# Kernel optimization log

Measured on AMD Instinct MI355X. Metric: run time of the kernel, lower is better.

The kernel has to match this reference:

```python
import jax, jax.numpy as jnp
import numpy as np

NPOINTS = 1024
RADIUS = 0.2
NSAMPLE = 32


def setup_inputs() -> dict:
    key = jax.random.key(0)
    k1, k2, k3, k4 = jax.random.split(key, 4)
    return {
        "xyz_all": jax.random.uniform(k1, (4, 8192, 3), jnp.float32),
        "normals": jax.random.normal(k2, (4, 8192, 3), jnp.float32),
        "xyz_voxel": jax.random.uniform(k3, (4, 4096, 3), jnp.float32),
        "normals_voxel": jax.random.normal(k4, (4, 4096, 3), jnp.float32),
    }


def _fps(xyz, npoints):
    # Furthest point sampling over a single cloud. xyz: (n, 3) -> (npoints,) int32
    n = xyz.shape[0]

    def body(carry, _):
        dists, last = carry
        d = jnp.sum((xyz - xyz[last]) ** 2, axis=-1)      # (n,) dist^2 to last pick
        dists = jnp.minimum(dists, d)                      # running min dist to set
        nxt = jnp.argmax(dists).astype(jnp.int32)          # farthest point
        return (dists, nxt), nxt

    init = (jnp.full((n,), 1e10, xyz.dtype), jnp.int32(0))
    _, rest = jax.lax.scan(body, init, None, length=npoints - 1)
    return jnp.concatenate([jnp.zeros((1,), jnp.int32), rest])


def _ball_query(xyz, new_xyz, radius, nsample):
    # xyz: (N,3) cloud, new_xyz: (S,3) centers -> (S, nsample) int32 indices
    # squared distances via GEMM form (compute-friendly)
    d2 = (jnp.sum(new_xyz ** 2, -1)[:, None] + jnp.sum(xyz ** 2, -1)[None, :]
          - 2.0 * jnp.einsum('sc,nc->sn', new_xyz, xyz))   # (S, N)
    N = xyz.shape[0]
    cand = jnp.where(d2 < radius * radius, jnp.arange(N, dtype=jnp.int32), N)
    cand = jnp.sort(cand, axis=-1)[:, :nsample]            # first nsample in-ball indices
    first = cand[:, :1]
    idx = jnp.where(cand == N, first, cand)                # pad with first valid index
    return jnp.where(idx == N, 0, idx)                     # degenerate: empty ball -> 0


def reference(xyz_all, normals, xyz_voxel, normals_voxel):
    # FPS on voxel points
    fps_idx = jax.vmap(lambda p: _fps(p, NPOINTS))(xyz_voxel)                 # (B, S)
    new_xyz = jax.vmap(lambda p, i: p[i])(xyz_voxel, fps_idx)                 # (B, S, 3)
    new_normals = jax.vmap(lambda p, i: p[i])(normals_voxel, fps_idx)         # (B, S, 3)
    # Ball query on full cloud
    idx = jax.vmap(lambda p, q: _ball_query(p, q, RADIUS, NSAMPLE))(xyz_all, new_xyz)  # (B, S, ns)
    grouped_xyz = jax.vmap(lambda p, i: p[i])(xyz_all, idx)                   # (B, S, ns, 3)
    rel = grouped_xyz - new_xyz[:, :, None, :]                                # center-relative
    new_features = jnp.transpose(rel, (0, 3, 1, 2))                           # (B, 3, S, ns)
    grouped_n = jax.vmap(lambda f, i: f[i])(normals, idx)                     # (B, S, ns, C)
    new_features_normals = jnp.concatenate(
        [new_features, jnp.transpose(grouped_n, (0, 3, 1, 2))], axis=1)       # (B, 3+C, S, ns)
    return new_xyz, new_normals, new_features, new_features_normals
```

## Files before the change

kernel.cpp:

```cpp
#include <hip/hip_runtime.h>
#include <hip/hip_bf16.h>

#define B 4
#define N_ALL 8192
#define N_VOX 4096
#define S_PTS 1024
#define K_SAMPLE 32
#define R2 0.04f

#define FPS_T 256
#define NPAIR 8
#define PREP_BLOCKS ((B * N_ALL) / FPS_T)

typedef float vf2 __attribute__((ext_vector_type(2)));

__device__ __forceinline__ double mk_key(float v, unsigned int ilo) {
    return __longlong_as_double(
        ((unsigned long long)__float_as_uint(v) << 32) | ilo);
}

__device__ __forceinline__ double wave_key_max_f64(double k) {
    unsigned long long ku = __double_as_longlong(k);
#define DPP_RED(ctrl)                                                              \
    {                                                                              \
        unsigned int lo = (unsigned int)ku;                                        \
        unsigned int hi = (unsigned int)(ku >> 32);                                \
        unsigned int nlo =                                                         \
            (unsigned int)__builtin_amdgcn_update_dpp(0, (int)lo, ctrl, 0xf, 0xf, false); \
        unsigned int nhi =                                                         \
            (unsigned int)__builtin_amdgcn_update_dpp(0, (int)hi, ctrl, 0xf, 0xf, false); \
        double nk = __longlong_as_double(((unsigned long long)nhi << 32) | nlo);   \
        double cur = fmax(__longlong_as_double(ku), nk);                           \
        ku = __double_as_longlong(cur);                                            \
    }
    DPP_RED(0x111);
    DPP_RED(0x112);
    DPP_RED(0x114);
    DPP_RED(0x118);
    DPP_RED(0x142);
    DPP_RED(0x143);
#undef DPP_RED
    return __longlong_as_double(ku);
}

__global__ __launch_bounds__(FPS_T, 1) void fps_prep_kernel(
    const float* __restrict__ xyz_voxel,
    const float* __restrict__ normals_voxel,
    const float* __restrict__ xyz_all,
    float* __restrict__ out_xyz,
    float* __restrict__ out_normals,
    float4* __restrict__ ws_packed,
    int do_prep)
{
#pragma clang fp contract(off)
    if (blockIdx.x >= B) {
        if (!do_prep) return;
        int pid = (blockIdx.x - B) * FPS_T + threadIdx.x;
        if (pid < B * N_ALL) {
            float x = xyz_all[pid * 3 + 0];
            float y = xyz_all[pid * 3 + 1];
            float z = xyz_all[pid * 3 + 2];
            float pp = __fadd_rn(__fadd_rn(__fmul_rn(x, x), __fmul_rn(y, y)),
                                 __fmul_rn(z, z));
            ws_packed[pid] = make_float4(x, y, z, pp);
        }
        return;
    }

    const int b = blockIdx.x;
    const int t = threadIdx.x;
    const int wid = t >> 6;
    const int lane = t & 63;

    __shared__ float4 sp[N_VOX];
    __shared__ int fps_idx_s[S_PTS];
    __shared__ alignas(16) unsigned long long s_part[2][FPS_T / 64];

    const float* xyz = xyz_voxel + (size_t)b * N_VOX * 3;
    for (int i = t; i < N_VOX; i += FPS_T) {
        float x = xyz[i * 3 + 0];
        float y = xyz[i * 3 + 1];
        float z = xyz[i * 3 + 2];
        sp[i] = make_float4(x, y, z, 0.0f);
    }
    __syncthreads();

    vf2 px2[NPAIR], py2[NPAIR], pz2[NPAIR], dist2[NPAIR];
    unsigned int ilo[2 * NPAIR];
#pragma unroll
    for (int jp = 0; jp < NPAIR; jp++) {
        float4 a = sp[t + (2 * jp) * FPS_T];
        float4 c = sp[t + (2 * jp + 1) * FPS_T];
        px2[jp] = vf2{a.x, c.x};
        py2[jp] = vf2{a.y, c.y};
        pz2[jp] = vf2{a.z, c.z};
        dist2[jp] = vf2{1e10f, 1e10f};
        ilo[2 * jp]     = ~(unsigned int)((2 * jp) * FPS_T + t);
        ilo[2 * jp + 1] = ~(unsigned int)((2 * jp + 1) * FPS_T + t);
    }

    if (t == 0) fps_idx_s[0] = 0;
    float4 c0 = sp[0];
    float lx = c0.x, ly = c0.y, lz = c0.z;

    for (int step = 1; step < S_PTS; step++) {
        double kk[2 * NPAIR];
#pragma unroll
        for (int jp = 0; jp < NPAIR; jp++) {
            vf2 dx = px2[jp] - lx;
            vf2 dy = py2[jp] - ly;
            vf2 dz = pz2[jp] - lz;
            vf2 d = (dx * dx + dy * dy) + dz * dz;
            vf2 dm = dist2[jp];
            dm.x = fminf(dm.x, d.x);
            dm.y = fminf(dm.y, d.y);
            dist2[jp] = dm;
            kk[2 * jp]     = mk_key(dm.x, ilo[2 * jp]);
            kk[2 * jp + 1] = mk_key(dm.y, ilo[2 * jp + 1]);
        }
        double m0 = fmax(fmax(kk[0], kk[1]),   fmax(kk[2], kk[3]));
        double m1 = fmax(fmax(kk[4], kk[5]),   fmax(kk[6], kk[7]));
        double m2 = fmax(fmax(kk[8], kk[9]),   fmax(kk[10], kk[11]));
        double m3 = fmax(fmax(kk[12], kk[13]), fmax(kk[14], kk[15]));
        double a0 = fmax(fmax(m0, m1), fmax(m2, m3));
        a0 = wave_key_max_f64(a0);

        const int buf = step & 1;
        if (lane == 63)
            s_part[buf][wid] = (unsigned long long)__double_as_longlong(a0);
        __syncthreads();
        double2 q0 = *((const double2*)&s_part[buf][0]);
        double2 q1 = *((const double2*)&s_part[buf][2]);
        double p0 = fmax(fmax(q0.x, q0.y), fmax(q1.x, q1.y));
        int besti = (int)(~(unsigned int)(unsigned long long)__double_as_longlong(p0))
                    & (N_VOX - 1);
        float4 cb = sp[besti];
        lx = cb.x; ly = cb.y; lz = cb.z;
        if (t == 0) fps_idx_s[step] = besti;
    }
    __syncthreads();

    for (int i = t; i < S_PTS; i += FPS_T) {
        int idx = fps_idx_s[i];
        int o = (b * S_PTS + i) * 3;
        float4 c = sp[idx];
        out_xyz[o + 0] = c.x;
        out_xyz[o + 1] = c.y;
        out_xyz[o + 2] = c.z;
        const float* nv = normals_voxel + ((size_t)b * N_VOX + idx) * 3;
        out_normals[o + 0] = nv[0];
        out_normals[o + 1] = nv[1];
        out_normals[o + 2] = nv[2];
    }
}

template <bool PACKED>
__global__ __launch_bounds__(256) void ballquery_group_kernel(
    const float* __restrict__ xyz_all,
    const float* __restrict__ normals,
    const float* __restrict__ new_xyz,
    const float4* __restrict__ pw,
    float* __restrict__ out_feat,
    float* __restrict__ out_featn)
{
#pragma clang fp contract(off)
    const int wid = threadIdx.x >> 6;
    const int lane = threadIdx.x & 63;
    const int q = blockIdx.x * 4 + wid;
    const int b = q >> 10;
    const int s = q & 1023;

    const float* xyz = xyz_all + (size_t)b * N_ALL * 3;
    const float* nrm = normals + (size_t)b * N_ALL * 3;
    const float4* pwb = PACKED ? (pw + (size_t)b * N_ALL) : nullptr;

    const float qx = new_xyz[q * 3 + 0];
    const float qy = new_xyz[q * 3 + 1];
    const float qz = new_xyz[q * 3 + 2];
    const float qq = __fadd_rn(__fadd_rn(__fmul_rn(qx, qx), __fmul_rn(qy, qy)),
                               __fmul_rn(qz, qz));

    __shared__ int sidx[4][K_SAMPLE];

    int cnt = 0;
    if (PACKED) {
        for (int g = 0; g < N_ALL / 256 && cnt < K_SAMPLE; g++) {
            int base = g * 256 + lane;
            float4 c0 = pwb[base];
            float4 c1 = pwb[base + 64];
            float4 c2 = pwb[base + 128];
            float4 c3 = pwb[base + 192];
            vf2 pxA = vf2{c0.x, c1.x}, pxB = vf2{c2.x, c3.x};
            vf2 pyA = vf2{c0.y, c1.y}, pyB = vf2{c2.y, c3.y};
            vf2 pzA = vf2{c0.z, c1.z}, pzB = vf2{c2.z, c3.z};
            vf2 ppA = vf2{c0.w, c1.w}, ppB = vf2{c2.w, c3.w};
            vf2 dtA = qx * pxA; dtA = dtA + qy * pyA; dtA = dtA + qz * pzA;
            vf2 dtB = qx * pxB; dtB = dtB + qy * pyB; dtB = dtB + qz * pzB;
            vf2 d2A = (qq + ppA) - 2.0f * dtA;
            vf2 d2B = (qq + ppB) - 2.0f * dtB;
            float d2s[4] = {d2A.x, d2A.y, d2B.x, d2B.y};
#pragma unroll
            for (int u = 0; u < 4; u++) {
                bool hit = d2s[u] < R2;
                unsigned long long mask = __ballot(hit);
                if (hit) {
                    int pos = cnt + __popcll(mask & ((1ull << lane) - 1ull));
                    if (pos < K_SAMPLE) sidx[wid][pos] = g * 256 + u * 64 + lane;
                }
                cnt += (int)__popcll(mask);
            }
        }
    } else {
        for (int c = 0; c < N_ALL / 64 && cnt < K_SAMPLE; c++) {
            int i = c * 64 + lane;
            float px = xyz[i * 3 + 0];
            float py = xyz[i * 3 + 1];
            float pz = xyz[i * 3 + 2];
            float pp = __fadd_rn(__fadd_rn(__fmul_rn(px, px), __fmul_rn(py, py)),
                                 __fmul_rn(pz, pz));
            float dt = __fadd_rn(__fadd_rn(__fmul_rn(qx, px), __fmul_rn(qy, py)),
                                 __fmul_rn(qz, pz));
            float d2 = __fsub_rn(__fadd_rn(qq, pp), __fmul_rn(2.0f, dt));
            bool hit = d2 < R2;
            unsigned long long mask = __ballot(hit);
            if (hit) {
                int pos = cnt + __popcll(mask & ((1ull << lane) - 1ull));
                if (pos < K_SAMPLE) sidx[wid][pos] = i;
            }
            cnt += (int)__popcll(mask);
        }
    }
    __syncthreads();

    if (lane < K_SAMPLE) {
        int idxj;
        if (cnt == 0)        idxj = 0;
        else if (lane < cnt) idxj = sidx[wid][lane];
        else                 idxj = sidx[wid][0];

        float px, py, pz;
        if (PACKED) {
            float4 cc = pwb[idxj];
            px = cc.x; py = cc.y; pz = cc.z;
        } else {
            px = xyz[idxj * 3 + 0];
            py = xyz[idxj * 3 + 1];
            pz = xyz[idxj * 3 + 2];
        }
        float rx = __fsub_rn(px, qx);
        float ry = __fsub_rn(py, qy);
        float rz = __fsub_rn(pz, qz);

        int o3 = ((b * 3) * S_PTS + s) * K_SAMPLE + lane;
        out_feat[o3 + 0 * 32768] = rx;
        out_feat[o3 + 1 * 32768] = ry;
        out_feat[o3 + 2 * 32768] = rz;

        float nx = nrm[idxj * 3 + 0];
        float ny = nrm[idxj * 3 + 1];
        float nz = nrm[idxj * 3 + 2];

        int o4 = ((b * 6) * S_PTS + s) * K_SAMPLE + lane;
        out_featn[o4 + 0 * 32768] = rx;
        out_featn[o4 + 1 * 32768] = ry;
        out_featn[o4 + 2 * 32768] = rz;
        out_featn[o4 + 3 * 32768] = nx;
        out_featn[o4 + 4 * 32768] = ny;
        out_featn[o4 + 5 * 32768] = nz;
    }
}

extern "C" void kernel_launch(void* const* d_in, const int* in_sizes, int n_in,
                              void* d_out, int out_size, void* d_ws, size_t ws_size,
                              hipStream_t stream) {
    const float* xyz_all       = (const float*)d_in[0];
    const float* normals       = (const float*)d_in[1];
    const float* xyz_voxel     = (const float*)d_in[2];
    const float* normals_voxel = (const float*)d_in[3];

    float* out = (float*)d_out;
    float* out_xyz     = out;
    float* out_normals = out + 12288;
    float* out_feat    = out + 24576;
    float* out_featn   = out + 417792;

    const size_t need = (size_t)B * N_ALL * sizeof(float4);
    const bool use_ws = ws_size >= need;

    fps_prep_kernel<<<B + (use_ws ? PREP_BLOCKS : 0), FPS_T, 0, stream>>>(
        xyz_voxel, normals_voxel, xyz_all, out_xyz, out_normals,
        (float4*)d_ws, use_ws ? 1 : 0);

    if (use_ws) {
        ballquery_group_kernel<true><<<(B * S_PTS) / 4, 256, 0, stream>>>(
            xyz_all, normals, out_xyz, (const float4*)d_ws, out_feat, out_featn);
    } else {
        ballquery_group_kernel<false><<<(B * S_PTS) / 4, 256, 0, stream>>>(
            xyz_all, normals, out_xyz, nullptr, out_feat, out_featn);
    }
}
```

Baseline: 583.1 us.

## Fuse FPS and ball query into one producer-consumer kernel

```diff
diff --git a/kernel.cpp b/kernel.cpp
--- a/kernel.cpp
+++ b/kernel.cpp
@@ -1,5 +1,4 @@
 #include <hip/hip_runtime.h>
-#include <hip/hip_bf16.h>
 
 #define B 4
 #define N_ALL 8192
@@ -10,7 +9,8 @@
 
 #define FPS_T 256
 #define NPAIR 8
-#define PREP_BLOCKS ((B * N_ALL) / FPS_T)
+#define CONS_BLOCKS 256
+#define PUB_CHUNK 128
 
 typedef float vf2 __attribute__((ext_vector_type(2)));
 
@@ -43,38 +43,149 @@
     return __longlong_as_double(ku);
 }
 
-__global__ __launch_bounds__(FPS_T, 1) void fps_prep_kernel(
+template <bool WAIT>
+__device__ void consumer_body(
+    const int W,
+    const float* __restrict__ xyz_all,
+    const float* __restrict__ normals,
+    const float* __restrict__ xyz_voxel,
+    const float* __restrict__ normals_voxel,
+    float* __restrict__ out_xyz,
+    float* __restrict__ out_normals,
+    float* __restrict__ out_feat,
+    float* __restrict__ out_featn,
+    const int* __restrict__ g_idx,
+    const int* __restrict__ prog,
+    int (*__restrict__ sidx)[K_SAMPLE])
+{
+#pragma clang fp contract(off)
+    const int wid = threadIdx.x >> 6;
+    const int lane = threadIdx.x & 63;
+    const int s = W;
+
+    if constexpr (WAIT) {
+        const int need = s + 1;
+        for (int b = 0; b < B; b++) {
+            int cur;
+            while ((cur = __hip_atomic_load(&prog[b], __ATOMIC_RELAXED,
+                                            __HIP_MEMORY_SCOPE_AGENT)) < need) {
+                if (need - cur > 2 * PUB_CHUNK) __builtin_amdgcn_s_sleep(127);
+                else                            __builtin_amdgcn_s_sleep(32);
+            }
+        }
+        __threadfence();
+    }
+
+    for (int b = 0; b < B; b++) {
+        const float* xyz = xyz_all + (size_t)b * N_ALL * 3;
+        const float* nrm = normals + (size_t)b * N_ALL * 3;
+
+        float qx, qy, qz;
+        if constexpr (WAIT) {
+            const int idx = g_idx[b * S_PTS + s];
+            const float* pv = xyz_voxel + ((size_t)b * N_VOX + idx) * 3;
+            const float* nv = normals_voxel + ((size_t)b * N_VOX + idx) * 3;
+            qx = pv[0]; qy = pv[1]; qz = pv[2];
+            if (lane < 3) {
+                out_xyz[(b * S_PTS + s) * 3 + lane]     = pv[lane];
+                out_normals[(b * S_PTS + s) * 3 + lane] = nv[lane];
+            }
+        } else {
+            const float* pv = out_xyz + (b * S_PTS + s) * 3;
+            qx = pv[0]; qy = pv[1]; qz = pv[2];
+        }
+        const float qq = __fadd_rn(__fadd_rn(__fmul_rn(qx, qx), __fmul_rn(qy, qy)),
+                                   __fmul_rn(qz, qz));
+
+        int cnt = 0;
+        for (int c = 0; c < N_ALL / 64 && cnt < K_SAMPLE; c++) {
+            const int i = c * 64 + lane;
+            const float px = xyz[i * 3 + 0];
+            const float py = xyz[i * 3 + 1];
+            const float pz = xyz[i * 3 + 2];
+            const float pp = __fadd_rn(__fadd_rn(__fmul_rn(px, px), __fmul_rn(py, py)),
+                                       __fmul_rn(pz, pz));
+            const float dt = __fadd_rn(__fadd_rn(__fmul_rn(qx, px), __fmul_rn(qy, py)),
+                                       __fmul_rn(qz, pz));
+            const float d2 = __fsub_rn(__fadd_rn(qq, pp), __fmul_rn(2.0f, dt));
+            const bool hit = d2 < R2;
+            const unsigned long long mask = __ballot(hit);
+            if (hit) {
+                int pos = cnt + __popcll(mask & ((1ull << lane) - 1ull));
+                if (pos < K_SAMPLE) sidx[wid][pos] = i;
+            }
+            cnt += (int)__popcll(mask);
+        }
+        __syncthreads();
+
+        if (lane < K_SAMPLE) {
+            int idxj;
+            if (cnt == 0)        idxj = 0;
+            else if (lane < cnt) idxj = sidx[wid][lane];
+            else                 idxj = sidx[wid][0];
+
+            const float px = xyz[idxj * 3 + 0];
+            const float py = xyz[idxj * 3 + 1];
+            const float pz = xyz[idxj * 3 + 2];
+            const float rx = __fsub_rn(px, qx);
+            const float ry = __fsub_rn(py, qy);
+            const float rz = __fsub_rn(pz, qz);
+
+            const int o3 = ((b * 3) * S_PTS + s) * K_SAMPLE + lane;
+            out_feat[o3 + 0 * 32768] = rx;
+            out_feat[o3 + 1 * 32768] = ry;
+            out_feat[o3 + 2 * 32768] = rz;
+
+            const float nx = nrm[idxj * 3 + 0];
+            const float ny = nrm[idxj * 3 + 1];
+            const float nz = nrm[idxj * 3 + 2];
+
+            const int o4 = ((b * 6) * S_PTS + s) * K_SAMPLE + lane;
+            out_featn[o4 + 0 * 32768] = rx;
+            out_featn[o4 + 1 * 32768] = ry;
+            out_featn[o4 + 2 * 32768] = rz;
+            out_featn[o4 + 3 * 32768] = nx;
+            out_featn[o4 + 4 * 32768] = ny;
+            out_featn[o4 + 5 * 32768] = nz;
+        }
+        __syncthreads();
+    }
+}
+
+template <bool OVERLAP>
+__global__ __launch_bounds__(FPS_T, 1) void fused_fps_bq_kernel(
     const float* __restrict__ xyz_voxel,
     const float* __restrict__ normals_voxel,
     const float* __restrict__ xyz_all,
+    const float* __restrict__ normals,
     float* __restrict__ out_xyz,
     float* __restrict__ out_normals,
-    float4* __restrict__ ws_packed,
-    int do_prep)
+    float* __restrict__ out_feat,
+    float* __restrict__ out_featn,
+    int* __restrict__ g_idx,
+    int* __restrict__ prog)
 {
 #pragma clang fp contract(off)
+    __shared__ float4 sp[N_VOX];
+    __shared__ int fps_idx_s[S_PTS];
+    __shared__ alignas(16) unsigned long long s_part[2][FPS_T / 64];
+    __shared__ int sidx[4][K_SAMPLE];
+
     if (blockIdx.x >= B) {
-        if (!do_prep) return;
-        int pid = (blockIdx.x - B) * FPS_T + threadIdx.x;
-        if (pid < B * N_ALL) {
-            float x = xyz_all[pid * 3 + 0];
-            float y = xyz_all[pid * 3 + 1];
-            float z = xyz_all[pid * 3 + 2];
-            float pp = __fadd_rn(__fadd_rn(__fmul_rn(x, x), __fmul_rn(y, y)),
-                                 __fmul_rn(z, z));
-            ws_packed[pid] = make_float4(x, y, z, pp);
-        }
+        consumer_body<true>((blockIdx.x - B) * 4 + (threadIdx.x >> 6),
+                            xyz_all, normals, xyz_voxel, normals_voxel,
+                            out_xyz, out_normals, out_feat, out_featn,
+                            g_idx, prog, sidx);
         return;
     }
+
+    __builtin_amdgcn_s_setprio(1);
 
     const int b = blockIdx.x;
     const int t = threadIdx.x;
     const int wid = t >> 6;
     const int lane = t & 63;
-
-    __shared__ float4 sp[N_VOX];
-    __shared__ int fps_idx_s[S_PTS];
-    __shared__ alignas(16) unsigned long long s_part[2][FPS_T / 64];
+    const int boff = b * S_PTS;
 
     const float* xyz = xyz_voxel + (size_t)b * N_VOX * 3;
     for (int i = t; i < N_VOX; i += FPS_T) {
@@ -99,7 +210,10 @@
         ilo[2 * jp + 1] = ~(unsigned int)((2 * jp + 1) * FPS_T + t);
     }
 
-    if (t == 0) fps_idx_s[0] = 0;
+    if (t == 0) {
+        fps_idx_s[0] = 0;
+        if constexpr (OVERLAP) g_idx[boff] = 0;
+    }
     float4 c0 = sp[0];
     float lx = c0.x, ly = c0.y, lz = c0.z;
 
@@ -136,138 +250,51 @@
                     & (N_VOX - 1);
         float4 cb = sp[besti];
         lx = cb.x; ly = cb.y; lz = cb.z;
-        if (t == 0) fps_idx_s[step] = besti;
-    }
-    __syncthreads();
-
-    for (int i = t; i < S_PTS; i += FPS_T) {
-        int idx = fps_idx_s[i];
-        int o = (b * S_PTS + i) * 3;
-        float4 c = sp[idx];
-        out_xyz[o + 0] = c.x;
-        out_xyz[o + 1] = c.y;
-        out_xyz[o + 2] = c.z;
-        const float* nv = normals_voxel + ((size_t)b * N_VOX + idx) * 3;
-        out_normals[o + 0] = nv[0];
-        out_normals[o + 1] = nv[1];
-        out_normals[o + 2] = nv[2];
-    }
-}
-
-template <bool PACKED>
-__global__ __launch_bounds__(256) void ballquery_group_kernel(
+        if (t == 0) {
+            fps_idx_s[step] = besti;
+            if constexpr (OVERLAP) {
+                g_idx[boff + step] = besti;
+                if ((step & (PUB_CHUNK - 1)) == (PUB_CHUNK - 1)) {
+                    __threadfence();
+                    __hip_atomic_store(&prog[b], step + 1, __ATOMIC_RELAXED,
+                                       __HIP_MEMORY_SCOPE_AGENT);
+                }
+            }
+        }
+    }
+
+    if constexpr (!OVERLAP) {
+        __syncthreads();
+        for (int i = t; i < S_PTS; i += FPS_T) {
+            int idx = fps_idx_s[i];
+            int o = (b * S_PTS + i) * 3;
+            float4 c = sp[idx];
+            out_xyz[o + 0] = c.x;
+            out_xyz[o + 1] = c.y;
+            out_xyz[o + 2] = c.z;
+            const float* nv = normals_voxel + ((size_t)b * N_VOX + idx) * 3;
+            out_normals[o + 0] = nv[0];
+            out_normals[o + 1] = nv[1];
+            out_normals[o + 2] = nv[2];
+        }
+    }
+}
+
+__global__ __launch_bounds__(256) void ballquery_fallback_kernel(
     const float* __restrict__ xyz_all,
     const float* __restrict__ normals,
-    const float* __restrict__ new_xyz,
-    const float4* __restrict__ pw,
+    const float* __restrict__ xyz_voxel,
+    const float* __restrict__ normals_voxel,
+    float* __restrict__ out_xyz,
+    float* __restrict__ out_normals,
     float* __restrict__ out_feat,
     float* __restrict__ out_featn)
 {
-#pragma clang fp contract(off)
-    const int wid = threadIdx.x >> 6;
-    const int lane = threadIdx.x & 63;
-    const int q = blockIdx.x * 4 + wid;
-    const int b = q >> 10;
-    const int s = q & 1023;
-
-    const float* xyz = xyz_all + (size_t)b * N_ALL * 3;
-    const float* nrm = normals + (size_t)b * N_ALL * 3;
-    const float4* pwb = PACKED ? (pw + (size_t)b * N_ALL) : nullptr;
-
-    const float qx = new_xyz[q * 3 + 0];
-    const float qy = new_xyz[q * 3 + 1];
-    const float qz = new_xyz[q * 3 + 2];
-    const float qq = __fadd_rn(__fadd_rn(__fmul_rn(qx, qx), __fmul_rn(qy, qy)),
-                               __fmul_rn(qz, qz));
-
     __shared__ int sidx[4][K_SAMPLE];
-
-    int cnt = 0;
-    if (PACKED) {
-        for (int g = 0; g < N_ALL / 256 && cnt < K_SAMPLE; g++) {
-            int base = g * 256 + lane;
-            float4 c0 = pwb[base];
-            float4 c1 = pwb[base + 64];
-            float4 c2 = pwb[base + 128];
-            float4 c3 = pwb[base + 192];
-            vf2 pxA = vf2{c0.x, c1.x}, pxB = vf2{c2.x, c3.x};
-            vf2 pyA = vf2{c0.y, c1.y}, pyB = vf2{c2.y, c3.y};
-            vf2 pzA = vf2{c0.z, c1.z}, pzB = vf2{c2.z, c3.z};
-            vf2 ppA = vf2{c0.w, c1.w}, ppB = vf2{c2.w, c3.w};
-            vf2 dtA = qx * pxA; dtA = dtA + qy * pyA; dtA = dtA + qz * pzA;
-            vf2 dtB = qx * pxB; dtB = dtB + qy * pyB; dtB = dtB + qz * pzB;
-            vf2 d2A = (qq + ppA) - 2.0f * dtA;
-            vf2 d2B = (qq + ppB) - 2.0f * dtB;
-            float d2s[4] = {d2A.x, d2A.y, d2B.x, d2B.y};
-#pragma unroll
-            for (int u = 0; u < 4; u++) {
-                bool hit = d2s[u] < R2;
-                unsigned long long mask = __ballot(hit);
-                if (hit) {
-                    int pos = cnt + __popcll(mask & ((1ull << lane) - 1ull));
-                    if (pos < K_SAMPLE) sidx[wid][pos] = g * 256 + u * 64 + lane;
-                }
-                cnt += (int)__popcll(mask);
-            }
-        }
-    } else {
-        for (int c = 0; c < N_ALL / 64 && cnt < K_SAMPLE; c++) {
-            int i = c * 64 + lane;
-            float px = xyz[i * 3 + 0];
-            float py = xyz[i * 3 + 1];
-            float pz = xyz[i * 3 + 2];
-            float pp = __fadd_rn(__fadd_rn(__fmul_rn(px, px), __fmul_rn(py, py)),
-                                 __fmul_rn(pz, pz));
-            float dt = __fadd_rn(__fadd_rn(__fmul_rn(qx, px), __fmul_rn(qy, py)),
-                                 __fmul_rn(qz, pz));
-            float d2 = __fsub_rn(__fadd_rn(qq, pp), __fmul_rn(2.0f, dt));
-            bool hit = d2 < R2;
-            unsigned long long mask = __ballot(hit);
-            if (hit) {
-                int pos = cnt + __popcll(mask & ((1ull << lane) - 1ull));
-                if (pos < K_SAMPLE) sidx[wid][pos] = i;
-            }
-            cnt += (int)__popcll(mask);
-        }
-    }
-    __syncthreads();
-
-    if (lane < K_SAMPLE) {
-        int idxj;
-        if (cnt == 0)        idxj = 0;
-        else if (lane < cnt) idxj = sidx[wid][lane];
-        else                 idxj = sidx[wid][0];
-
-        float px, py, pz;
-        if (PACKED) {
-            float4 cc = pwb[idxj];
-            px = cc.x; py = cc.y; pz = cc.z;
-        } else {
-            px = xyz[idxj * 3 + 0];
-            py = xyz[idxj * 3 + 1];
-            pz = xyz[idxj * 3 + 2];
-        }
-        float rx = __fsub_rn(px, qx);
-        float ry = __fsub_rn(py, qy);
-        float rz = __fsub_rn(pz, qz);
-
-        int o3 = ((b * 3) * S_PTS + s) * K_SAMPLE + lane;
-        out_feat[o3 + 0 * 32768] = rx;
-        out_feat[o3 + 1 * 32768] = ry;
-        out_feat[o3 + 2 * 32768] = rz;
-
-        float nx = nrm[idxj * 3 + 0];
-        float ny = nrm[idxj * 3 + 1];
-        float nz = nrm[idxj * 3 + 2];
-
-        int o4 = ((b * 6) * S_PTS + s) * K_SAMPLE + lane;
-        out_featn[o4 + 0 * 32768] = rx;
-        out_featn[o4 + 1 * 32768] = ry;
-        out_featn[o4 + 2 * 32768] = rz;
-        out_featn[o4 + 3 * 32768] = nx;
-        out_featn[o4 + 4 * 32768] = ny;
-        out_featn[o4 + 5 * 32768] = nz;
-    }
+    consumer_body<false>(blockIdx.x * 4 + (threadIdx.x >> 6),
+                         xyz_all, normals, xyz_voxel, normals_voxel,
+                         out_xyz, out_normals, out_feat, out_featn,
+                         nullptr, nullptr, sidx);
 }
 
 extern "C" void kernel_launch(void* const* d_in, const int* in_sizes, int n_in,
@@ -284,18 +311,22 @@
     float* out_feat    = out + 24576;
     float* out_featn   = out + 417792;
 
-    const size_t need = (size_t)B * N_ALL * sizeof(float4);
+    const size_t need = (size_t)B * S_PTS * sizeof(int) + B * sizeof(int);
     const bool use_ws = ws_size >= need;
 
-    fps_prep_kernel<<<B + (use_ws ? PREP_BLOCKS : 0), FPS_T, 0, stream>>>(
-        xyz_voxel, normals_voxel, xyz_all, out_xyz, out_normals,
-        (float4*)d_ws, use_ws ? 1 : 0);
-
     if (use_ws) {
-        ballquery_group_kernel<true><<<(B * S_PTS) / 4, 256, 0, stream>>>(
-            xyz_all, normals, out_xyz, (const float4*)d_ws, out_feat, out_featn);
+        int* g_idx = (int*)d_ws;
+        int* prog  = g_idx + B * S_PTS;
+        hipMemsetAsync(prog, 0, B * sizeof(int), stream);
+        fused_fps_bq_kernel<true><<<B + CONS_BLOCKS, FPS_T, 0, stream>>>(
+            xyz_voxel, normals_voxel, xyz_all, normals,
+            out_xyz, out_normals, out_feat, out_featn, g_idx, prog);
     } else {
-        ballquery_group_kernel<false><<<(B * S_PTS) / 4, 256, 0, stream>>>(
-            xyz_all, normals, out_xyz, nullptr, out_feat, out_featn);
-    }
-}
+        fused_fps_bq_kernel<false><<<B, FPS_T, 0, stream>>>(
+            xyz_voxel, normals_voxel, xyz_all, normals,
+            out_xyz, out_normals, out_feat, out_featn, nullptr, nullptr);
+        ballquery_fallback_kernel<<<CONS_BLOCKS, 256, 0, stream>>>(
+            xyz_all, normals, xyz_voxel, normals_voxel,
+            out_xyz, out_normals, out_feat, out_featn);
+    }
+}
```

Measured after the change: 613.7 us. 1.05x slower.

## Replace per-step FPS block barrier with tagged shared-memory spin-wait records

Applied to the files above, without the earlier changes.

```diff
diff --git a/kernel.cpp b/kernel.cpp
--- a/kernel.cpp
+++ b/kernel.cpp
@@ -1,5 +1,4 @@
 #include <hip/hip_runtime.h>
-#include <hip/hip_bf16.h>
 
 #define B 4
 #define N_ALL 8192
@@ -74,7 +73,12 @@
 
     __shared__ float4 sp[N_VOX];
     __shared__ int fps_idx_s[S_PTS];
-    __shared__ alignas(16) unsigned long long s_part[2][FPS_T / 64];
+    __shared__ alignas(16) ulonglong2 s_rec[2][4];
+
+    if (t < 8) {
+        ulonglong2 z2; z2.x = 0ull; z2.y = 0ull;
+        s_rec[t >> 2][t & 3] = z2;
+    }
 
     const float* xyz = xyz_voxel + (size_t)b * N_VOX * 3;
     for (int i = t; i < N_VOX; i += FPS_T) {
@@ -126,12 +130,30 @@
         a0 = wave_key_max_f64(a0);
 
         const int buf = step & 1;
-        if (lane == 63)
-            s_part[buf][wid] = (unsigned long long)__double_as_longlong(a0);
-        __syncthreads();
-        double2 q0 = *((const double2*)&s_part[buf][0]);
-        double2 q1 = *((const double2*)&s_part[buf][2]);
-        double p0 = fmax(fmax(q0.x, q0.y), fmax(q1.x, q1.y));
+        if (lane == 63) {
+            ulonglong2 rec;
+            rec.x = (unsigned long long)__double_as_longlong(a0);
+            rec.y = (unsigned long long)(unsigned int)step;
+            s_rec[buf][wid] = rec;
+        }
+
+        const unsigned long long tgt = (unsigned long long)(unsigned int)step;
+        double p0;
+        for (;;) {
+            asm volatile("" ::: "memory");
+            ulonglong2 r0 = s_rec[buf][0];
+            ulonglong2 r1 = s_rec[buf][1];
+            ulonglong2 r2 = s_rec[buf][2];
+            ulonglong2 r3 = s_rec[buf][3];
+            if ((((r0.y ^ tgt) | (r1.y ^ tgt)) | ((r2.y ^ tgt) | (r3.y ^ tgt))) == 0ull) {
+                double k0 = __longlong_as_double((long long)r0.x);
+                double k1 = __longlong_as_double((long long)r1.x);
+                double k2 = __longlong_as_double((long long)r2.x);
+                double k3 = __longlong_as_double((long long)r3.x);
+                p0 = fmax(fmax(k0, k1), fmax(k2, k3));
+                break;
+            }
+        }
         int besti = (int)(~(unsigned int)(unsigned long long)__double_as_longlong(p0))
                     & (N_VOX - 1);
         float4 cb = sp[besti];
```

Result: slower. 659.2 us (+13.1%).
